# Performance work log

Measured on AMD Instinct MI355X. Metric: run time of the kernel, lower is better.

Reference implementation:

```python
import jax, jax.numpy as jnp
import numpy as np

N, E, EMB, G, L = 30000, 480000, 256, 512, 3
AVOCAB, BVOCAB, EDIM = 128, 16, 3
NEG_SLOPE = 0.2


def setup_inputs() -> dict:
    key = jax.random.key(0)
    ks = jax.random.split(key, 20)
    s = 0.05
    x = jax.random.randint(ks[0], (N, 9), 0, AVOCAB)
    edge_index = jax.random.randint(ks[1], (2, E), 0, N)
    edge_attr = jax.random.randint(ks[2], (E, 3), 0, BVOCAB)
    batch = jnp.sort(jax.random.randint(ks[3], (N,), 0, G))
    return {
        "x": x, "edge_index": edge_index, "edge_attr": edge_attr, "batch": batch,
        # AtomEncoder: 9 embedding tables summed -> [N, EMB]
        "atom_emb": jax.random.normal(ks[4], (9, AVOCAB, EMB)) * s,
        # BondEncoder per layer: 3 tables summed -> [E, 3]
        "bond_emb": jax.random.normal(ks[5], (L, 3, BVOCAB, EDIM)) * s,
        # GATConv per layer (heads=1): lin W, att vectors, lin_edge, bias
        "W": jax.random.normal(ks[6], (L, EMB, EMB)) * s,
        "att_src": jax.random.normal(ks[7], (L, EMB)) * s,
        "att_dst": jax.random.normal(ks[8], (L, EMB)) * s,
        "We": jax.random.normal(ks[9], (L, EDIM, EMB)) * s,
        "att_edge": jax.random.normal(ks[10], (L, EMB)) * s,
        "bias": jnp.zeros((L, EMB)),
        # head MLP: Linear(EMB,EMB) -> Linear(EMB,1), no activation between
        "W1": jax.random.normal(ks[11], (EMB, EMB)) * s,
        "b1": jnp.zeros((EMB,)),
        "W2": jax.random.normal(ks[12], (EMB, 1)) * s,
        "b2": jnp.zeros((1,)),
    }


def _gat_conv(h, src, dst, e_enc, W, a_s, a_d, We, a_e, b):
    # PyG GATConv, heads=1, add_self_loops=True, fill_value='mean'.
    # self-loop edge_attr = mean of incoming edge attrs per node (0 if none)
    deg = jax.ops.segment_sum(jnp.ones((E,), h.dtype), dst, num_segments=N)
    loop_attr = jax.ops.segment_sum(e_enc, dst, num_segments=N) / jnp.clip(deg, 1.0)[:, None]
    e_all = jnp.concatenate([e_enc, loop_attr], axis=0)          # [E+N, 3]
    loops = jnp.arange(N, dtype=src.dtype)
    src_a = jnp.concatenate([src, loops])
    dst_a = jnp.concatenate([dst, loops])
    xl = h @ W                                                    # [N, C]
    alpha = (xl @ a_s)[src_a] + (xl @ a_d)[dst_a] + (e_all @ We) @ a_e  # [E+N]
    alpha = jnp.where(alpha >= 0, alpha, NEG_SLOPE * alpha)       # leaky_relu
    # segment softmax over destination (every node has a self loop -> nonempty)
    m = jax.ops.segment_max(alpha, dst_a, num_segments=N)
    p = jnp.exp(alpha - m[dst_a])
    denom = jax.ops.segment_sum(p, dst_a, num_segments=N)
    w = p / denom[dst_a]
    out = jax.ops.segment_sum(w[:, None] * xl[src_a], dst_a, num_segments=N)
    return out + b


def reference(x, edge_index, edge_attr, batch, atom_emb, bond_emb, W, att_src,
              att_dst, We, att_edge, bias, W1, b1, W2, b2):
    src, dst = edge_index[0], edge_index[1]
    # AtomEncoder: sum of 9 feature embeddings
    h = sum(atom_emb[i][x[:, i]] for i in range(9))               # [N, EMB]
    for l in range(L):
        e_enc = sum(bond_emb[l, j][edge_attr[:, j]] for j in range(3))  # [E, 3]
        hc = _gat_conv(h, src, dst, e_enc, W[l], att_src[l], att_dst[l],
                       We[l], att_edge[l], bias[l])
        if l < L - 1:
            hc = jax.nn.relu(hc)
        h = hc + h  # residual (dropout is identity in eval)
    # global mean pool
    cnt = jax.ops.segment_sum(jnp.ones((N,), h.dtype), batch, num_segments=G)
    hg = jax.ops.segment_sum(h, batch, num_segments=G) / jnp.clip(cnt, 1.0)[:, None]
    return (hg @ W1 + b1) @ W2 + b2                               # [G, 1]
```

## Files before the change

### kernel.cpp

```cpp
#include <hip/hip_runtime.h>
#include <hip/hip_bf16.h>

#define NN   30000
#define NE   480000
#define EMBD 256
#define NG   512
#define NLAY 3
#define LEAK 0.2f
#define NBLK_SCAN 118
#define GROWS 48

typedef __attribute__((ext_vector_type(8))) short bf16x8;
typedef __attribute__((ext_vector_type(4))) float f32x4;
typedef __attribute__((ext_vector_type(4))) unsigned short us4;
typedef __attribute__((ext_vector_type(8))) unsigned short us8;

__device__ __forceinline__ float bf2f(unsigned short u) {
  union { unsigned int i; float f; } v; v.i = ((unsigned int)u) << 16; return v.f;
}
__device__ __forceinline__ unsigned short f2bf(float f) {
  union { float f; unsigned int i; } v; v.f = f;
  unsigned int u = v.i;
  u += 0x7fffu + ((u >> 16) & 1u);
  return (unsigned short)(u >> 16);
}
__device__ __forceinline__ float rdw(const void* p, size_t i, int f32) {
  return f32 ? ((const float*)p)[i] : bf2f(((const unsigned short*)p)[i]);
}

__global__ __launch_bounds__(256) void k_sniff_hist(const unsigned short* __restrict__ w,
                                                    int* cnt, const int* __restrict__ dst,
                                                    int* cnt_i) {
  int b = blockIdx.x;
  if (b < 16) {
    __shared__ int sh;
    if (threadIdx.x == 0) sh = 0;
    __syncthreads();
    int local = 0;
    for (int i = (b * 256 + threadIdx.x) * 2; i < 65536; i += 16 * 256 * 2) {
      unsigned short u = w[i];
      if (((u >> 7) & 0xFF) == 0xFF) local++;
    }
    atomicAdd(&sh, local);
    __syncthreads();
    if (threadIdx.x == 0 && sh) atomicAdd(cnt, sh);
  } else {
    int e = (b - 16) * 256 + threadIdx.x;
    if (e < NE) atomicAdd(&cnt_i[dst[e]], 1);
  }
}

__global__ __launch_bounds__(256) void k_scan_dots(const int* __restrict__ cnt_i,
                                                   int* row_ptr, int* part,
                                                   const void* __restrict__ We,
                                                   const void* __restrict__ ae,
                                                   const void* __restrict__ W1,
                                                   const void* __restrict__ b1,
                                                   const void* __restrict__ W2,
                                                   const void* __restrict__ b2,
                                                   const int* __restrict__ cntp,
                                                   float* __restrict__ wa_all,
                                                   float* __restrict__ v,
                                                   float* __restrict__ c0) {
  int b = blockIdx.x;
  if (b < NBLK_SCAN) {
    __shared__ int sh[256];
    int t = threadIdx.x;
    int i = b * 256 + t;
    int val = (i < NN) ? cnt_i[i] : 0;
    sh[t] = val;
    __syncthreads();
    for (int off = 1; off < 256; off <<= 1) {
      int tmp = (t >= off) ? sh[t - off] : 0;
      __syncthreads();
      sh[t] += tmp;
      __syncthreads();
    }
    if (i < NN) row_ptr[i] = sh[t] - val;
    if (t == 255) part[b] = sh[255];
  } else {
    int f32 = (*cntp >= 4) ? 1 : 0;
    int wid  = (b - NBLK_SCAN) * 4 + (threadIdx.x >> 6);
    int lane = threadIdx.x & 63;
    if (wid >= 266) return;
    float s = 0.f;
    if (wid < 256) {
      for (int c = lane; c < 256; c += 64)
        s += rdw(W1, (size_t)wid*256 + c, f32) * rdw(W2, c, f32);
    } else if (wid < 265) {
      int t = wid - 256;
      int l = t / 3, j = t % 3;
      for (int c = lane; c < 256; c += 64)
        s += rdw(We, (size_t)l*768 + j*256 + c, f32) * rdw(ae, (size_t)l*256 + c, f32);
    } else {
      for (int c = lane; c < 256; c += 64)
        s += rdw(b1, c, f32) * rdw(W2, c, f32);
    }
    #pragma unroll
    for (int o = 32; o > 0; o >>= 1) s += __shfl_down(s, o);
    if (lane == 0) {
      if (wid < 256)      v[wid] = s;
      else if (wid < 265) wa_all[wid - 256] = s;
      else                *c0 = s + rdw(b2, 0, f32);
    }
  }
}

__global__ __launch_bounds__(128) void k_scan_mid(const int* __restrict__ part,
                                                  int* __restrict__ offs) {
  __shared__ int sh[128];
  int t = threadIdx.x;
  int v = (t < NBLK_SCAN) ? part[t] : 0;
  sh[t] = v;
  __syncthreads();
  for (int off = 1; off < 128; off <<= 1) {
    int tmp = (t >= off) ? sh[t - off] : 0;
    __syncthreads();
    sh[t] += tmp;
    __syncthreads();
  }
  if (t < NBLK_SCAN) offs[t] = sh[t] - v;
}

__global__ void k_scan_add(int* row_ptr, const int* __restrict__ offs, int* cursor) {
  int b = blockIdx.x, t = threadIdx.x;
  int i = b * 256 + t;
  if (i < NN) {
    int v = row_ptr[i] + offs[b];
    row_ptr[i] = v;
    cursor[i]  = v;
  }
  if (i == 0) row_ptr[NN] = NE;
}

__global__ void k_fill(const int* __restrict__ src, const int* __restrict__ dst,
                       int* cursor, int* col_src, int* col_eid) {
  int e = blockIdx.x * 256 + threadIdx.x;
  if (e >= NE) return;
  int pos = atomicAdd(&cursor[dst[e]], 1);
  col_src[pos] = src[e];
  col_eid[pos] = e;
}

__global__ __launch_bounds__(256) void k_atom_prep(const int* __restrict__ x,
                                                   const void* __restrict__ emb,
                                                   float* __restrict__ h,
                                                   unsigned short* __restrict__ hbf,
                                                   const void* __restrict__ W,
                                                   unsigned short* __restrict__ Wt,
                                                   const int* __restrict__ cntp) {
  int f32 = (*cntp >= 4) ? 1 : 0;
  int b = blockIdx.x;
  if (b < NN) {
    int c = threadIdx.x;
    float s = 0.f;
    #pragma unroll
    for (int i = 0; i < 9; ++i) {
      int xi = x[b * 9 + i];
      s += rdw(emb, (size_t)(i * 128 + xi) * 256 + c, f32);
    }
    h[(size_t)b * 256 + c] = s;
    hbf[(size_t)b * 256 + c] = f2bf(s);
  } else {
    int t = (b - NN) * 256 + threadIdx.x;
    int l = t >> 16;
    int k = (t >> 8) & 255;
    int c = t & 255;
    Wt[(l << 16) + (c << 8) + k] = f2bf(rdw(W, t, f32));
  }
}

__global__ __launch_bounds__(256) void k_we(const int* __restrict__ eattr,
                                            const int* __restrict__ col_eid,
                                            const void* __restrict__ bemb,
                                            const float* __restrict__ wa_all,
                                            float* __restrict__ we_csr,
                                            const int* __restrict__ cntp) {
  int f32 = (*cntp >= 4) ? 1 : 0;
  int j = blockIdx.x * 256 + threadIdx.x;
  if (j >= NE) return;
  int e = col_eid[j];
  int a0 = eattr[e*3], a1 = eattr[e*3+1], a2 = eattr[e*3+2];
  #pragma unroll
  for (int l = 0; l < NLAY; ++l) {
    size_t lb = (size_t)l * 144;
    float e0 = rdw(bemb, lb + (0*16+a0)*3+0, f32) + rdw(bemb, lb + (1*16+a1)*3+0, f32)
             + rdw(bemb, lb + (2*16+a2)*3+0, f32);
    float e1 = rdw(bemb, lb + (0*16+a0)*3+1, f32) + rdw(bemb, lb + (1*16+a1)*3+1, f32)
             + rdw(bemb, lb + (2*16+a2)*3+1, f32);
    float e2 = rdw(bemb, lb + (0*16+a0)*3+2, f32) + rdw(bemb, lb + (1*16+a1)*3+2, f32)
             + rdw(bemb, lb + (2*16+a2)*3+2, f32);
    we_csr[(size_t)l*NE + j] = e0*wa_all[l*3+0] + e1*wa_all[l*3+1] + e2*wa_all[l*3+2];
  }
}


__global__ __launch_bounds__(256) void k_gemm_fused(const unsigned short* __restrict__ A,
                                                    const unsigned short* __restrict__ Bt,
                                                    const void* __restrict__ as_w,
                                                    const void* __restrict__ ad_w, int l,
                                                    unsigned short* __restrict__ xlbf,
                                                    float* __restrict__ as_,
                                                    float* __restrict__ ad_,
                                                    const int* __restrict__ cntp) {
  __shared__ unsigned short xtile[GROWS][256];
  __shared__ float sred[4][3][16], dred[4][3][16];
  int b = blockIdx.x;
  int w = threadIdx.x >> 6;
  int lane = threadIdx.x & 63;
  int m0 = b * GROWS;
  int c0 = w * 64;
  int lr = lane & 15;
  int g  = lane >> 4;
  int lk = g * 8;
  f32x4 acc[3][4];
  #pragma unroll
  for (int rg = 0; rg < 3; ++rg)
    #pragma unroll
    for (int q = 0; q < 4; ++q) acc[rg][q] = (f32x4){0.f,0.f,0.f,0.f};

  const unsigned short* brow  = Bt + (size_t)(c0 + lr) * 256 + lk;
  const unsigned short* arow0 = A  + (size_t)(m0 + lr) * 256 + lk;
  #pragma unroll
  for (int k = 0; k < 256; k += 32) {
    bf16x8 b0 = *(const bf16x8*)(brow + k);
    bf16x8 b1 = *(const bf16x8*)(brow + 16*256 + k);
    bf16x8 b2 = *(const bf16x8*)(brow + 32*256 + k);
    bf16x8 b3 = *(const bf16x8*)(brow + 48*256 + k);
    #pragma unroll
    for (int rg = 0; rg < 3; ++rg) {
      bf16x8 a = *(const bf16x8*)(arow0 + (size_t)rg*16*256 + k);
      acc[rg][0] = __builtin_amdgcn_mfma_f32_16x16x32_bf16(a, b0, acc[rg][0], 0,0,0);
      acc[rg][1] = __builtin_amdgcn_mfma_f32_16x16x32_bf16(a, b1, acc[rg][1], 0,0,0);
      acc[rg][2] = __builtin_amdgcn_mfma_f32_16x16x32_bf16(a, b2, acc[rg][2], 0,0,0);
      acc[rg][3] = __builtin_amdgcn_mfma_f32_16x16x32_bf16(a, b3, acc[rg][3], 0,0,0);
    }
  }
  int f32 = (*cntp >= 4) ? 1 : 0;
  float asw[4], adw[4];
  #pragma unroll
  for (int q = 0; q < 4; ++q) {
    asw[q] = rdw(as_w, (size_t)l*256 + c0 + 16*q + lr, f32);
    adw[q] = rdw(ad_w, (size_t)l*256 + c0 + 16*q + lr, f32);
  }
  #pragma unroll
  for (int rg = 0; rg < 3; ++rg) {
    #pragma unroll
    for (int r = 0; r < 4; ++r) {
      float sv = acc[rg][0][r]*asw[0] + acc[rg][1][r]*asw[1]
               + acc[rg][2][r]*asw[2] + acc[rg][3][r]*asw[3];
      float dv = acc[rg][0][r]*adw[0] + acc[rg][1][r]*adw[1]
               + acc[rg][2][r]*adw[2] + acc[rg][3][r]*adw[3];
      #pragma unroll
      for (int o = 1; o < 16; o <<= 1) { sv += __shfl_xor(sv, o); dv += __shfl_xor(dv, o); }
      if (lr == 0) { sred[w][rg][g*4+r] = sv; dred[w][rg][g*4+r] = dv; }
      int row = rg*16 + g*4 + r;
      xtile[row][c0 + lr +  0] = f2bf(acc[rg][0][r]);
      xtile[row][c0 + lr + 16] = f2bf(acc[rg][1][r]);
      xtile[row][c0 + lr + 32] = f2bf(acc[rg][2][r]);
      xtile[row][c0 + lr + 48] = f2bf(acc[rg][3][r]);
    }
  }
  __syncthreads();
  int t = threadIdx.x;
  if (t < GROWS) {
    int rg = t >> 4, rr = t & 15;
    float s = sred[0][rg][rr] + sred[1][rg][rr] + sred[2][rg][rr] + sred[3][rg][rr];
    float d = dred[0][rg][rr] + dred[1][rg][rr] + dred[2][rg][rr] + dred[3][rg][rr];
    as_[m0 + t] = s;
    ad_[m0 + t] = d;
  }
  {
    const us8* srcp = (const us8*)&xtile[0][0];
    us8* dstp = (us8*)(xlbf + (size_t)m0 * 256);
    #pragma unroll
    for (int u = 0; u < 6; ++u) dstp[t + u*256] = srcp[t + u*256];
  }
}

__global__ __launch_bounds__(256) void k_fused(const int* __restrict__ row_ptr,
                                               const int* __restrict__ col_src,
                                               const float* __restrict__ we_csr,
                                               const float* __restrict__ as_,
                                               const float* __restrict__ ad_,
                                               const unsigned short* __restrict__ xlbf,
                                               const void* __restrict__ bias, int l,
                                               float* __restrict__ h,
                                               unsigned short* __restrict__ hbf,
                                               int do_relu, const int* __restrict__ cntp) {
  int n = blockIdx.x * 4 + (threadIdx.x >> 6);
  int lane = threadIdx.x & 63;
  int beg = row_ptr[n], end = row_ptr[n+1];
  int deg = end - beg;
  float ad_n = ad_[n];

  float dsum_l = 0.f, wesum_l = 0.f;
  float ax = 0.f, ay = 0.f, az = 0.f, aw = 0.f;

  for (int cb = beg; cb < end; cb += 64) {
    int j = cb + lane;
    bool valid = (j < end);
    int s = valid ? col_src[j] : 0;
    float we = valid ? we_csr[j] : 0.f;
    wesum_l += we;
    float p = 0.f;
    if (valid) {
      float a = as_[s] + ad_n + we;
      a = (a >= 0.f) ? a : LEAK * a;
      p = __expf(fmaxf(fminf(a, 60.f), -60.f));
    }
    dsum_l += p;
    int cl = end - cb; if (cl > 64) cl = 64;
    #pragma unroll 4
    for (int jj = 0; jj < cl; ++jj) {
      float ww = __shfl(p, jj);
      int   ss = __shfl(s, jj);
      us4 xv = *(const us4*)(xlbf + (size_t)ss*256 + lane*4);
      ax += ww*bf2f(xv.x); ay += ww*bf2f(xv.y);
      az += ww*bf2f(xv.z); aw += ww*bf2f(xv.w);
    }
  }
  #pragma unroll
  for (int o = 32; o > 0; o >>= 1) {
    dsum_l  += __shfl_xor(dsum_l, o);
    wesum_l += __shfl_xor(wesum_l, o);
  }

  float a_self = as_[n] + ad_n + wesum_l / fmaxf((float)deg, 1.f);
  a_self = (a_self >= 0.f) ? a_self : LEAK * a_self;
  float p_self = __expf(fmaxf(fminf(a_self, 60.f), -60.f));
  float dsum = dsum_l + p_self;
  {
    us4 xv = *(const us4*)(xlbf + (size_t)n*256 + lane*4);
    ax += p_self*bf2f(xv.x); ay += p_self*bf2f(xv.y);
    az += p_self*bf2f(xv.z); aw += p_self*bf2f(xv.w);
  }
  float inv_d = 1.f / dsum;
  ax *= inv_d; ay *= inv_d; az *= inv_d; aw *= inv_d;

  int f32 = (*cntp >= 4) ? 1 : 0;
  int c0 = lane * 4;
  ax += rdw(bias, (size_t)l*256 + c0+0, f32);
  ay += rdw(bias, (size_t)l*256 + c0+1, f32);
  az += rdw(bias, (size_t)l*256 + c0+2, f32);
  aw += rdw(bias, (size_t)l*256 + c0+3, f32);
  if (do_relu) {
    ax = fmaxf(ax, 0.f); ay = fmaxf(ay, 0.f);
    az = fmaxf(az, 0.f); aw = fmaxf(aw, 0.f);
  }
  float* hp = h + (size_t)n*256 + c0;
  float4 hv = *(const float4*)hp;
  float h0 = ax + hv.x, h1 = ay + hv.y, h2 = az + hv.z, h3 = aw + hv.w;
  *(float4*)hp = make_float4(h0, h1, h2, h3);
  us4 q = { f2bf(h0), f2bf(h1), f2bf(h2), f2bf(h3) };
  *(us4*)(hbf + (size_t)n*256 + c0) = q;
}


__global__ __launch_bounds__(256) void k_pool_head(const float* __restrict__ h,
                                                   const int* __restrict__ batch,
                                                   const float* __restrict__ v,
                                                   const float* __restrict__ c0,
                                                   void* __restrict__ out,
                                                   const int* __restrict__ cntp) {
  int g = blockIdx.x;
  int lo = 0, hi = NN;
  while (lo < hi) { int mid = (lo + hi) >> 1; if (batch[mid] < g) lo = mid + 1; else hi = mid; }
  int start = lo;
  lo = 0; hi = NN;
  while (lo < hi) { int mid = (lo + hi) >> 1; if (batch[mid] < g + 1) lo = mid + 1; else hi = mid; }
  int endn = lo;

  int c = threadIdx.x;
  float s = 0.f;
  for (int n = start; n < endn; ++n) s += h[(size_t)n*256 + c];
  __shared__ float red[256];
  red[c] = s * v[c];
  __syncthreads();
  for (int off = 128; off > 0; off >>= 1) {
    if (c < off) red[c] += red[c + off];
    __syncthreads();
  }
  if (c == 0) {
    float cntf = (float)(endn - start);
    float val = red[0] / fmaxf(cntf, 1.f) + *c0;
    if (*cntp >= 4) ((float*)out)[g] = val;
    else            ((unsigned short*)out)[g] = f2bf(val);
  }
}

extern "C" void kernel_launch(void* const* d_in, const int* in_sizes, int n_in,
                              void* d_out, int out_size, void* d_ws, size_t ws_size,
                              hipStream_t stream) {
  const int* x     = (const int*)d_in[0];
  const int* eidx  = (const int*)d_in[1];
  const int* eattr = (const int*)d_in[2];
  const int* batch = (const int*)d_in[3];
  const void* atom_emb = d_in[4];
  const void* bond_emb = d_in[5];
  const void* W        = d_in[6];
  const void* att_src  = d_in[7];
  const void* att_dst  = d_in[8];
  const void* We       = d_in[9];
  const void* att_edge = d_in[10];
  const void* bias     = d_in[11];
  const void* W1 = d_in[12];
  const void* b1 = d_in[13];
  const void* W2 = d_in[14];
  const void* b2 = d_in[15];

  const int* src = eidx;
  const int* dst = eidx + NE;

  char* base = (char*)d_ws;
  size_t off = 0;
  auto alloc = [&](size_t bytes) -> char* {
    char* p = base + off; off += (bytes + 255) & ~(size_t)255; return p;
  };
  float* h    = (float*)alloc((size_t)NN*EMBD*4);
  unsigned short* xlbf = (unsigned short*)alloc((size_t)NN*EMBD*2);
  unsigned short* hbf  = (unsigned short*)alloc((size_t)NN*EMBD*2);
  unsigned short* wt   = (unsigned short*)alloc((size_t)NLAY*EMBD*EMBD*2);
  float* we_csr = (float*)alloc((size_t)NLAY*NE*4);
  float* as_   = (float*)alloc((size_t)NN*4);
  float* ad_   = (float*)alloc((size_t)NN*4);
  float* vvec  = (float*)alloc((size_t)EMBD*4);
  float* c0    = (float*)alloc(4);
  float* wa_all= (float*)alloc(64);
  int*   cnt   = (int*)alloc(4);
  int* cnt_i   = (int*)alloc((size_t)NN*4);
  int* row_ptr = (int*)alloc((size_t)(NN+1)*4);
  int* cursor  = (int*)alloc((size_t)NN*4);
  int* col_src = (int*)alloc((size_t)NE*4);
  int* col_eid = (int*)alloc((size_t)NE*4);
  int* part    = (int*)alloc((size_t)NBLK_SCAN*4);
  int* offs    = (int*)alloc((size_t)NBLK_SCAN*4);

  (void)hipMemsetAsync(cnt, 0, 4, stream);
  (void)hipMemsetAsync(cnt_i, 0, (size_t)NN*4, stream);
  k_sniff_hist<<<16 + (NE+255)/256, 256, 0, stream>>>((const unsigned short*)atom_emb,
                                                      cnt, dst, cnt_i);
  k_scan_dots<<<NBLK_SCAN + 67, 256, 0, stream>>>(cnt_i, row_ptr, part,
                                                  We, att_edge, W1, b1, W2, b2,
                                                  cnt, wa_all, vvec, c0);
  k_scan_mid<<<1, 128, 0, stream>>>(part, offs);
  k_scan_add<<<NBLK_SCAN, 256, 0, stream>>>(row_ptr, offs, cursor);
  k_fill<<<(NE+255)/256, 256, 0, stream>>>(src, dst, cursor, col_src, col_eid);
  k_atom_prep<<<NN + 768, 256, 0, stream>>>(x, atom_emb, h, hbf, W, wt, cnt);
  k_we<<<(NE+255)/256, 256, 0, stream>>>(eattr, col_eid, bond_emb, wa_all, we_csr, cnt);

  for (int l = 0; l < NLAY; ++l) {
    k_gemm_fused<<<NN/GROWS, 256, 0, stream>>>(hbf, wt + (size_t)l*EMBD*EMBD,
                                               att_src, att_dst, l, xlbf, as_, ad_, cnt);
    k_fused<<<NN/4, 256, 0, stream>>>(row_ptr, col_src, we_csr + (size_t)l*NE,
                                      as_, ad_, xlbf, bias, l, h, hbf,
                                      (l < NLAY-1) ? 1 : 0, cnt);
  }

  k_pool_head<<<NG, 256, 0, stream>>>(h, batch, vvec, c0, d_out, cnt);
}
```

Before: 452.0 us.

## Drop fp32 residual buffer, fuse edge-weight compute into CSR fill, prefetch edges

Removes the fp32 copy of the node features. The residual update and the pooling now read and write only the bf16 buffer, which cuts global memory traffic in the fused aggregation and pooling kernels. The per-edge bond-attention weights are now computed inside the CSR fill kernel, which drops the separate k_we kernel and the col_eid indirection. The aggregation loop also prefetches the next chunk of edge indices and weights. The cost is that the residual is accumulated in bf16 across layers, which loses precision.

```diff
diff --git a/kernel.cpp b/kernel.cpp
--- a/kernel.cpp
+++ b/kernel.cpp
@@ -133,18 +133,32 @@
   if (i == 0) row_ptr[NN] = NE;
 }
 
-__global__ void k_fill(const int* __restrict__ src, const int* __restrict__ dst,
-                       int* cursor, int* col_src, int* col_eid) {
+__global__ void k_fill_we(const int* __restrict__ src, const int* __restrict__ dst,
+                          const int* __restrict__ eattr, const void* __restrict__ bemb,
+                          const float* __restrict__ wa_all, int* cursor,
+                          int* col_src, float* __restrict__ we_csr,
+                          const int* __restrict__ cntp) {
   int e = blockIdx.x * 256 + threadIdx.x;
   if (e >= NE) return;
+  int f32 = (*cntp >= 4) ? 1 : 0;
   int pos = atomicAdd(&cursor[dst[e]], 1);
   col_src[pos] = src[e];
-  col_eid[pos] = e;
+  int a0 = eattr[e*3], a1 = eattr[e*3+1], a2 = eattr[e*3+2];
+  #pragma unroll
+  for (int l = 0; l < NLAY; ++l) {
+    size_t lb = (size_t)l * 144;
+    float e0 = rdw(bemb, lb + (0*16+a0)*3+0, f32) + rdw(bemb, lb + (1*16+a1)*3+0, f32)
+             + rdw(bemb, lb + (2*16+a2)*3+0, f32);
+    float e1 = rdw(bemb, lb + (0*16+a0)*3+1, f32) + rdw(bemb, lb + (1*16+a1)*3+1, f32)
+             + rdw(bemb, lb + (2*16+a2)*3+1, f32);
+    float e2 = rdw(bemb, lb + (0*16+a0)*3+2, f32) + rdw(bemb, lb + (1*16+a1)*3+2, f32)
+             + rdw(bemb, lb + (2*16+a2)*3+2, f32);
+    we_csr[(size_t)l*NE + pos] = e0*wa_all[l*3+0] + e1*wa_all[l*3+1] + e2*wa_all[l*3+2];
+  }
 }
 
 __global__ __launch_bounds__(256) void k_atom_prep(const int* __restrict__ x,
                                                    const void* __restrict__ emb,
-                                                   float* __restrict__ h,
                                                    unsigned short* __restrict__ hbf,
                                                    const void* __restrict__ W,
                                                    unsigned short* __restrict__ Wt,
@@ -159,7 +173,6 @@
       int xi = x[b * 9 + i];
       s += rdw(emb, (size_t)(i * 128 + xi) * 256 + c, f32);
     }
-    h[(size_t)b * 256 + c] = s;
     hbf[(size_t)b * 256 + c] = f2bf(s);
   } else {
     int t = (b - NN) * 256 + threadIdx.x;
@@ -167,30 +180,6 @@
     int k = (t >> 8) & 255;
     int c = t & 255;
     Wt[(l << 16) + (c << 8) + k] = f2bf(rdw(W, t, f32));
-  }
-}
-
-__global__ __launch_bounds__(256) void k_we(const int* __restrict__ eattr,
-                                            const int* __restrict__ col_eid,
-                                            const void* __restrict__ bemb,
-                                            const float* __restrict__ wa_all,
-                                            float* __restrict__ we_csr,
-                                            const int* __restrict__ cntp) {
-  int f32 = (*cntp >= 4) ? 1 : 0;
-  int j = blockIdx.x * 256 + threadIdx.x;
-  if (j >= NE) return;
-  int e = col_eid[j];
-  int a0 = eattr[e*3], a1 = eattr[e*3+1], a2 = eattr[e*3+2];
-  #pragma unroll
-  for (int l = 0; l < NLAY; ++l) {
-    size_t lb = (size_t)l * 144;
-    float e0 = rdw(bemb, lb + (0*16+a0)*3+0, f32) + rdw(bemb, lb + (1*16+a1)*3+0, f32)
-             + rdw(bemb, lb + (2*16+a2)*3+0, f32);
-    float e1 = rdw(bemb, lb + (0*16+a0)*3+1, f32) + rdw(bemb, lb + (1*16+a1)*3+1, f32)
-             + rdw(bemb, lb + (2*16+a2)*3+1, f32);
-    float e2 = rdw(bemb, lb + (0*16+a0)*3+2, f32) + rdw(bemb, lb + (1*16+a1)*3+2, f32)
-             + rdw(bemb, lb + (2*16+a2)*3+2, f32);
-    we_csr[(size_t)l*NE + j] = e0*wa_all[l*3+0] + e1*wa_all[l*3+1] + e2*wa_all[l*3+2];
   }
 }
 
@@ -285,7 +274,6 @@
                                                const float* __restrict__ ad_,
                                                const unsigned short* __restrict__ xlbf,
                                                const void* __restrict__ bias, int l,
-                                               float* __restrict__ h,
                                                unsigned short* __restrict__ hbf,
                                                int do_relu, const int* __restrict__ cntp) {
   int n = blockIdx.x * 4 + (threadIdx.x >> 6);
@@ -297,15 +285,19 @@
   float dsum_l = 0.f, wesum_l = 0.f;
   float ax = 0.f, ay = 0.f, az = 0.f, aw = 0.f;
 
+  int s_cur = 0; float we_cur = 0.f;
+  { int j = beg + lane; if (j < end) { s_cur = col_src[j]; we_cur = we_csr[j]; } }
+
   for (int cb = beg; cb < end; cb += 64) {
-    int j = cb + lane;
-    bool valid = (j < end);
-    int s = valid ? col_src[j] : 0;
-    float we = valid ? we_csr[j] : 0.f;
-    wesum_l += we;
+    int jn = cb + 64 + lane;
+    int s_nxt = 0; float we_nxt = 0.f;
+    if (jn < end) { s_nxt = col_src[jn]; we_nxt = we_csr[jn]; }
+
+    bool valid = (cb + lane) < end;
+    wesum_l += we_cur;
     float p = 0.f;
     if (valid) {
-      float a = as_[s] + ad_n + we;
+      float a = as_[s_cur] + ad_n + we_cur;
       a = (a >= 0.f) ? a : LEAK * a;
       p = __expf(fmaxf(fminf(a, 60.f), -60.f));
     }
@@ -314,11 +306,12 @@
     #pragma unroll 4
     for (int jj = 0; jj < cl; ++jj) {
       float ww = __shfl(p, jj);
-      int   ss = __shfl(s, jj);
+      int   ss = __shfl(s_cur, jj);
       us4 xv = *(const us4*)(xlbf + (size_t)ss*256 + lane*4);
       ax += ww*bf2f(xv.x); ay += ww*bf2f(xv.y);
       az += ww*bf2f(xv.z); aw += ww*bf2f(xv.w);
     }
+    s_cur = s_nxt; we_cur = we_nxt;
   }
   #pragma unroll
   for (int o = 32; o > 0; o >>= 1) {
@@ -348,16 +341,16 @@
     ax = fmaxf(ax, 0.f); ay = fmaxf(ay, 0.f);
     az = fmaxf(az, 0.f); aw = fmaxf(aw, 0.f);
   }
-  float* hp = h + (size_t)n*256 + c0;
-  float4 hv = *(const float4*)hp;
-  float h0 = ax + hv.x, h1 = ay + hv.y, h2 = az + hv.z, h3 = aw + hv.w;
-  *(float4*)hp = make_float4(h0, h1, h2, h3);
+  unsigned short* hp = hbf + (size_t)n*256 + c0;
+  us4 hv = *(const us4*)hp;
+  float h0 = ax + bf2f(hv.x), h1 = ay + bf2f(hv.y);
+  float h2 = az + bf2f(hv.z), h3 = aw + bf2f(hv.w);
   us4 q = { f2bf(h0), f2bf(h1), f2bf(h2), f2bf(h3) };
-  *(us4*)(hbf + (size_t)n*256 + c0) = q;
-}
-
-
-__global__ __launch_bounds__(256) void k_pool_head(const float* __restrict__ h,
+  *(us4*)hp = q;
+}
+
+
+__global__ __launch_bounds__(256) void k_pool_head(const unsigned short* __restrict__ hbf,
                                                    const int* __restrict__ batch,
                                                    const float* __restrict__ v,
                                                    const float* __restrict__ c0,
@@ -373,7 +366,7 @@
 
   int c = threadIdx.x;
   float s = 0.f;
-  for (int n = start; n < endn; ++n) s += h[(size_t)n*256 + c];
+  for (int n = start; n < endn; ++n) s += bf2f(hbf[(size_t)n*256 + c]);
   __shared__ float red[256];
   red[c] = s * v[c];
   __syncthreads();
@@ -417,7 +410,6 @@
   auto alloc = [&](size_t bytes) -> char* {
     char* p = base + off; off += (bytes + 255) & ~(size_t)255; return p;
   };
-  float* h    = (float*)alloc((size_t)NN*EMBD*4);
   unsigned short* xlbf = (unsigned short*)alloc((size_t)NN*EMBD*2);
   unsigned short* hbf  = (unsigned short*)alloc((size_t)NN*EMBD*2);
   unsigned short* wt   = (unsigned short*)alloc((size_t)NLAY*EMBD*EMBD*2);
@@ -432,7 +424,6 @@
   int* row_ptr = (int*)alloc((size_t)(NN+1)*4);
   int* cursor  = (int*)alloc((size_t)NN*4);
   int* col_src = (int*)alloc((size_t)NE*4);
-  int* col_eid = (int*)alloc((size_t)NE*4);
   int* part    = (int*)alloc((size_t)NBLK_SCAN*4);
   int* offs    = (int*)alloc((size_t)NBLK_SCAN*4);
 
@@ -445,17 +436,17 @@
                                                   cnt, wa_all, vvec, c0);
   k_scan_mid<<<1, 128, 0, stream>>>(part, offs);
   k_scan_add<<<NBLK_SCAN, 256, 0, stream>>>(row_ptr, offs, cursor);
-  k_fill<<<(NE+255)/256, 256, 0, stream>>>(src, dst, cursor, col_src, col_eid);
-  k_atom_prep<<<NN + 768, 256, 0, stream>>>(x, atom_emb, h, hbf, W, wt, cnt);
-  k_we<<<(NE+255)/256, 256, 0, stream>>>(eattr, col_eid, bond_emb, wa_all, we_csr, cnt);
+  k_fill_we<<<(NE+255)/256, 256, 0, stream>>>(src, dst, eattr, bond_emb, wa_all,
+                                              cursor, col_src, we_csr, cnt);
+  k_atom_prep<<<NN + 768, 256, 0, stream>>>(x, atom_emb, hbf, W, wt, cnt);
 
   for (int l = 0; l < NLAY; ++l) {
     k_gemm_fused<<<NN/GROWS, 256, 0, stream>>>(hbf, wt + (size_t)l*EMBD*EMBD,
                                                att_src, att_dst, l, xlbf, as_, ad_, cnt);
     k_fused<<<NN/4, 256, 0, stream>>>(row_ptr, col_src, we_csr + (size_t)l*NE,
-                                      as_, ad_, xlbf, bias, l, h, hbf,
+                                      as_, ad_, xlbf, bias, l, hbf,
                                       (l < NLAY-1) ? 1 : 0, cnt);
   }
 
-  k_pool_head<<<NG, 256, 0, stream>>>(h, batch, vvec, c0, d_out, cnt);
-}
+  k_pool_head<<<NG, 256, 0, stream>>>(hbf, batch, vvec, c0, d_out, cnt);
+}
```

Result: faster. 440.1 us (-2.6%).
